# Optimization experiments

Hardware: AMD Instinct MI355X
Metric: run time of the kernel (lower is better)

Reference implementation:

```python
import jax, jax.numpy as jnp
import numpy as np
import math

EPS = 1e-5

def _bn_lrelu(x, g, b, m, v):
    # BatchNorm2d (eval, running stats) + LeakyReLU(0.01)
    inv = jax.lax.rsqrt(v + EPS)
    xn = (x - m[None, :, None, None]) * (g * inv)[None, :, None, None] + b[None, :, None, None]
    return jnp.where(xn >= 0, xn, 0.01 * xn)

def _conv3x3(x, w, b):
    # zero pad 1 on freq (dim2) and time (dim3) (pad_left state is None -> zeros), valid 3x3 conv
    x = jnp.pad(x, ((0, 0), (0, 0), (1, 1), (1, 1)))
    y = jax.lax.conv_general_dilated(x, w, (1, 1), 'VALID',
                                     dimension_numbers=('NCHW', 'OIHW', 'NCHW'))
    return y + b[None, :, None, None]

def _conv1x1(x, w, b):
    return jnp.einsum('bcft,oc->boft', x, w[:, :, 0, 0]) + b[None, :, None, None]

def _blockx3(x, g, b, m, v, w, wb):
    return _conv3x3(_bn_lrelu(x, g, b, m, v), w, wb)

def _mha(x, wqkv, bqkv, wo, bo, n_heads=4, L=64, U=128):
    # banded local attention over time, window = (L back, L fwd), chunked by U
    B, C, F, T = x.shape
    H = n_heads; D = C // H; S = 2 * L
    qkv = _conv1x1(x, wqkv, bqkv)                 # [B,3C,F,T]
    qkv = qkv.transpose(0, 2, 1, 3)               # [B,F,3C,T]
    def split(a):
        return a.reshape(B * F, H, D, T).transpose(0, 1, 3, 2)  # [BF,H,T,D]
    q = split(qkv[:, :, :C])
    k = split(qkv[:, :, C:2 * C])
    v = split(qkv[:, :, 2 * C:])
    Tkv = T + L                                   # kv padded left by L (zero state)
    nC = T // U
    pad_to = nC * U + S                           # pad kv right so every chunk window exists
    kp = jnp.pad(k, ((0, 0), (0, 0), (L, pad_to - Tkv), (0, 0)))
    vp = jnp.pad(v, ((0, 0), (0, 0), (L, pad_to - Tkv), (0, 0)))
    idx = (jnp.arange(nC) * U)[:, None] + jnp.arange(U + S)[None, :]   # [nC, U+S]
    kc = kp[:, :, idx, :]                         # [BF,H,nC,U+S,D]
    vc = vp[:, :, idx, :]
    qc = q.reshape(B * F, H, nC, U, D)
    i = jnp.arange(U)[:, None]; j = jnp.arange(U + S)[None, :]
    band = (j >= i) & (j <= i + S)                # row i sees cols i..i+S (width 1+2L)
    valid = (jnp.arange(nC)[:, None] * U + jnp.arange(U + S)[None, :]) < Tkv
    mask = (band[None, :, :] & valid[:, None, :]).astype(x.dtype)      # [nC,U,U+S]
    scores = jnp.einsum('bhcqd,bhckd->bhcqk', qc, kc) / math.sqrt(D)
    scores = scores * mask - 10000.0 * (1.0 - mask)
    p = jax.nn.softmax(scores, axis=-1)
    o = jnp.einsum('bhcqk,bhckd->bhcqd', p, vc)   # [BF,H,nC,U,D]
    o = o.reshape(B * F, H, T, D).transpose(0, 1, 3, 2).reshape(B, F, C, T).transpose(0, 2, 1, 3)
    return _conv1x1(o, wo, bo)

def setup_inputs() -> dict:
    key = jax.random.key(0)
    ks = jax.random.split(key, 40)
    d = {}
    d['x'] = jax.random.normal(ks[0], (4, 64, 64, 512), dtype=jnp.float32)
    def bn(i, c, pre):
        d[pre + '_g'] = jax.random.normal(ks[i], (c,), jnp.float32) * 0.1 + 1.0
        d[pre + '_b'] = jax.random.normal(ks[i + 1], (c,), jnp.float32) * 0.1
        d[pre + '_m'] = jax.random.normal(ks[i + 2], (c,), jnp.float32) * 0.1
        d[pre + '_v'] = jax.random.uniform(ks[i + 3], (c,), jnp.float32, 0.5, 1.5)
    def conv(i, o, c, kh, kw, pre):
        fan = c * kh * kw
        d[pre + '_w'] = jax.random.normal(ks[i], (o, c, kh, kw), jnp.float32) / math.sqrt(fan)
        d[pre + '_wb'] = jax.random.normal(ks[i + 1], (o,), jnp.float32) * 0.01
    bn(1, 64, 'bd0');  conv(5, 32, 64, 3, 3, 'bd0')
    bn(7, 96, 'bd1');  conv(11, 32, 96, 3, 3, 'bd1')
    bn(13, 128, 'bdo'); conv(17, 64, 128, 3, 3, 'bdo')
    d['qkv_w'] = jax.random.normal(ks[19], (192, 64, 1, 1), jnp.float32) / math.sqrt(64)
    d['qkv_b'] = jax.random.normal(ks[20], (192,), jnp.float32) * 0.01
    d['o_w'] = jax.random.normal(ks[21], (64, 64, 1, 1), jnp.float32) / math.sqrt(64)
    d['o_b'] = jax.random.normal(ks[22], (64,), jnp.float32) * 0.01
    bn(23, 128, 'sao'); conv(27, 64, 128, 1, 1, 'sao')
    return d

def reference(x,
              bd0_g, bd0_b, bd0_m, bd0_v, bd0_w, bd0_wb,
              bd1_g, bd1_b, bd1_m, bd1_v, bd1_w, bd1_wb,
              bdo_g, bdo_b, bdo_m, bdo_v, bdo_w, bdo_wb,
              qkv_w, qkv_b, o_w, o_b,
              sao_g, sao_b, sao_m, sao_v, sao_w, sao_wb):
    # dense conv stack: 64 -> +32 -> +32 -> 64
    a0 = _blockx3(x, bd0_g, bd0_b, bd0_m, bd0_v, bd0_w, bd0_wb)
    x1 = jnp.concatenate([x, a0], axis=1)                 # [B,96,F,T]
    a1 = _blockx3(x1, bd1_g, bd1_b, bd1_m, bd1_v, bd1_w, bd1_wb)
    x2 = jnp.concatenate([x1, a1], axis=1)                # [B,128,F,T]
    y = _blockx3(x2, bdo_g, bdo_b, bdo_m, bdo_v, bdo_w, bdo_wb)  # [B,64,F,T]
    # banded self-attention branch
    att = _mha(y, qkv_w, qkv_b, o_w, o_b)                 # [B,64,F,T]
    z = jnp.concatenate([y, att], axis=1)                 # [B,128,F,T]
    out = _conv1x1(_bn_lrelu(z, sao_g, sao_b, sao_m, sao_v), sao_w, sao_wb)
    return out
```

## Files before the change

kernel.cpp:

```cpp
#include <hip/hip_runtime.h>
#include <hip/hip_bf16.h>

typedef unsigned short u16t;
typedef __attribute__((ext_vector_type(8))) short bfrag;
typedef __attribute__((ext_vector_type(4))) float f32x4;
typedef __attribute__((ext_vector_type(8))) unsigned short uh8;

__device__ __forceinline__ float bfu(u16t u) {
    union { unsigned int i; float f; } c;
    c.i = ((unsigned int)u) << 16;
    return c.f;
}
__device__ __forceinline__ u16t fbf(float f) {
    __hip_bfloat16 h = __float2bfloat16(f);
    return *reinterpret_cast<u16t*>(&h);
}
__device__ __forceinline__ unsigned int fbf2(float lo, float hi) {
    unsigned int r;
    asm("v_cvt_pk_bf16_f32 %0, %1, %2" : "=v"(r) : "v"(lo), "v"(hi));
    return r;
}
__device__ __forceinline__ float rcpf(float x) {
    float r;
    asm("v_rcp_f32 %0, %1" : "=v"(r) : "v"(x));
    return r;
}

__global__ __launch_bounds__(256) void prep_x3_k(
    const float* __restrict__ x,
    const float* __restrict__ g0, const float* __restrict__ b0,
    const float* __restrict__ m0, const float* __restrict__ v0,
    const float* __restrict__ g1, const float* __restrict__ b1,
    const float* __restrict__ m1, const float* __restrict__ v1,
    const float* __restrict__ g2, const float* __restrict__ b2,
    const float* __restrict__ m2, const float* __restrict__ v2,
    u16t* __restrict__ xn0, u16t* __restrict__ xn1, u16t* __restrict__ xn2)
{
    constexpr int F = 64, T = 512;
    __shared__ u16t su[64][74];
    __shared__ float ssc[3][64], ssh[3][64];
    const int tid = threadIdx.x;
    const int t0 = blockIdx.x * 64;
    const int f = blockIdx.y, b = blockIdx.z;

    if (tid < 64) {
        int c = tid;
        float s;
        s = g0[c] * rsqrtf(v0[c] + 1e-5f); ssc[0][c] = s; ssh[0][c] = b0[c] - m0[c] * s;
        s = g1[c] * rsqrtf(v1[c] + 1e-5f); ssc[1][c] = s; ssh[1][c] = b1[c] - m1[c] * s;
        s = g2[c] * rsqrtf(v2[c] + 1e-5f); ssc[2][c] = s; ssh[2][c] = b2[c] - m2[c] * s;
    }
#pragma unroll
    for (int p = 0; p < 16; p++) {
        int i = tid + 256 * p;
        int c = i >> 6, t = i & 63;
        su[c][t] = fbf(x[(((long)b * 64 + c) * F + f) * T + t0 + t]);
    }
    __syncthreads();
#pragma unroll
    for (int p = 0; p < 2; p++) {
        int i = tid + 256 * p;
        int t = i >> 3, c8 = i & 7;
        float n0[8], n1[8], n2[8];
#pragma unroll
        for (int j = 0; j < 8; j++) {
            int c = c8 * 8 + j;
            float xv = bfu(su[c][t]);
            float a0 = fmaf(xv, ssc[0][c], ssh[0][c]);
            float a1 = fmaf(xv, ssc[1][c], ssh[1][c]);
            float a2 = fmaf(xv, ssc[2][c], ssh[2][c]);
            n0[j] = fmaxf(a0, 0.01f * a0);
            n1[j] = fmaxf(a1, 0.01f * a1);
            n2[j] = fmaxf(a2, 0.01f * a2);
        }
        union { uh8 h; unsigned int w[4]; } u0, u1, u2;
#pragma unroll
        for (int j4 = 0; j4 < 4; j4++) {
            u0.w[j4] = fbf2(n0[j4 * 2], n0[j4 * 2 + 1]);
            u1.w[j4] = fbf2(n1[j4 * 2], n1[j4 * 2 + 1]);
            u2.w[j4] = fbf2(n2[j4 * 2], n2[j4 * 2 + 1]);
        }
        long gi = (((long)b * F + f) * T + t0 + t) * 64 + c8 * 8;
        *(uh8*)&xn0[gi] = u0.h;
        *(uh8*)&xn1[gi] = u1.h;
        *(uh8*)&xn2[gi] = u2.h;
    }
}

__global__ __launch_bounds__(256) void prep_w_k(
    const float* __restrict__ w0, const float* __restrict__ w1,
    const float* __restrict__ w2, const float* __restrict__ ow,
    const float* __restrict__ sw, const float* __restrict__ qw,
    u16t* __restrict__ wp)
{
    int idx = blockIdx.x * 256 + threadIdx.x;
    if (idx >= 144384) return;
    if (idx < 119808) {
        int C_IN, C_OUT, e;
        const float* src;
        if (idx < 18432)      { C_IN = 64;  C_OUT = 32; src = w0; e = idx; }
        else if (idx < 46080) { C_IN = 96;  C_OUT = 32; src = w1; e = idx - 18432; }
        else                  { C_IN = 128; C_OUT = 64; src = w2; e = idx - 46080; }
        int NCOT = C_OUT / 16;
        int j  = e & 7;
        int l  = (e >> 3) & 63;
        int r  = e >> 9;
        int ct = r % NCOT;
        int r2 = r / NCOT;
        int kk = r2 % 9;
        int cb = r2 / 9;
        int co  = ct * 16 + (l & 15);
        int kin = cb * 32 + (l >> 4) * 8 + j;
        int kh = kk / 3, kw = kk % 3;
        wp[idx] = fbf(src[((co * C_IN + kin) * 3 + kh) * 3 + kw]);
    } else if (idx < 123904) {
        int e = idx - 119808;
        int ks = e & 31, co = (e >> 5) & 63, kb = e >> 11;
        wp[idx] = fbf(ow[co * 64 + kb * 32 + ks]);
    } else if (idx < 132096) {
        int e = idx - 123904;
        int ks = e & 31, co = (e >> 5) & 63, kb = e >> 11;
        wp[idx] = fbf(sw[co * 128 + kb * 32 + ks]);
    } else {
        int e = idx - 132096;
        int ks = e & 31, co = (e >> 5) % 192, kb = e / 6144;
        wp[idx] = fbf(qw[co * 64 + kb * 32 + ks]);
    }
}

template<int C_IN, int C_OUT, int EPI>
__global__ __launch_bounds__(256) void conv3x3_ff4_k(
    const u16t* __restrict__ s0, const u16t* __restrict__ s1,
    const u16t* __restrict__ s2,
    const u16t* __restrict__ wseg, const float* __restrict__ wb,
    const float* __restrict__ g1, const float* __restrict__ b1,
    const float* __restrict__ m1, const float* __restrict__ v1,
    const float* __restrict__ g2, const float* __restrict__ b2,
    const float* __restrict__ m2, const float* __restrict__ v2,
    int bnoff, u16t* __restrict__ dst1, u16t* __restrict__ dst2)
{
    constexpr int F = 64, T = 512, TT = 64, FF = 4;
    constexpr int NCH  = C_IN / 32;
    constexpr int NCOT = C_OUT / 16;
    constexpr int WT = 9 * NCOT * 64;
    constexpr int XT = 6 * 66 * 4;

    __shared__ __align__(16) u16t s_x[6][66][40];
    __shared__ __align__(16) u16t s_w[WT * 8];

    const int tid = threadIdx.x;
    const int t0 = blockIdx.x * TT;
    const int f0 = blockIdx.y * FF;
    const int b  = blockIdx.z;

    const int l  = tid & 63;
    const int wv = tid >> 6;
    const int lr = l & 15;
    const int lq = l >> 4;

    f32x4 acc[4][NCOT];
#pragma unroll
    for (int i = 0; i < 4; i++)
#pragma unroll
        for (int j = 0; j < NCOT; j++) acc[i][j] = (f32x4){0.f, 0.f, 0.f, 0.f};

    for (int ch = 0; ch < NCH; ch++) {
        if (ch) __syncthreads();

        for (int idx = tid; idx < XT + WT; idx += 256) {
            if (idx < XT) {
                int oct = idx & 3;
                int row = idx >> 2;
                int fr = row / 66;
                int tp = row - fr * 66;
                int fi = f0 + fr - 1;
                int tg = t0 + tp - 1;
                int gc8 = ch * 4 + oct;
                uh8 v = (uh8)0;
                if ((unsigned)fi < (unsigned)F && (unsigned)tg < (unsigned)T) {
                    const u16t* sp; int coff, cw;
                    if (C_IN == 64 || gc8 < 8) { sp = s0; coff = gc8 * 8;        cw = 64; }
                    else if (gc8 < 12)         { sp = s1; coff = (gc8 - 8) * 8;  cw = 32; }
                    else                       { sp = s2; coff = (gc8 - 12) * 8; cw = 32; }
                    v = *(const uh8*)&sp[(((long)b * F + fi) * T + tg) * cw + coff];
                }
                *(uh8*)&s_x[fr][tp][oct * 8] = v;
            } else {
                int w = idx - XT;
                *(uh8*)&s_w[w * 8] = *(const uh8*)&wseg[((long)ch * WT + w) * 8];
            }
        }
        __syncthreads();

#pragma unroll
        for (int kk = 0; kk < 9; kk++) {
            const int kh = kk / 3, kw = kk % 3;
            bfrag A[NCOT];
#pragma unroll
            for (int ct = 0; ct < NCOT; ct++)
                A[ct] = *(const bfrag*)&s_w[((kk * NCOT + ct) * 64 + l) * 8];
#pragma unroll
            for (int ts = 0; ts < 4; ts++) {
                bfrag B = *(const bfrag*)&s_x[wv + kh][ts * 16 + lr + kw][lq * 8];
#pragma unroll
                for (int ct = 0; ct < NCOT; ct++)
                    acc[ts][ct] = __builtin_amdgcn_mfma_f32_16x16x32_bf16(
                        A[ct], B, acc[ts][ct], 0, 0, 0);
            }
        }
    }

    const int f = f0 + wv;
#pragma unroll
    for (int ct = 0; ct < NCOT; ct++) {
        const int co0 = ct * 16 + lq * 4;
        float4 bs = *(const float4*)&wb[co0];
        float sc1[4], sh1[4], sc2[4], sh2[4];
        if (EPI >= 1) {
#pragma unroll
            for (int j = 0; j < 4; j++) {
                int c = bnoff + co0 + j;
                float s = g1[c] * rsqrtf(v1[c] + 1e-5f);
                sc1[j] = s; sh1[j] = b1[c] - m1[c] * s;
            }
        }
        if (EPI == 2) {
#pragma unroll
            for (int j = 0; j < 4; j++) {
                int c = bnoff + co0 + j;
                float s = g2[c] * rsqrtf(v2[c] + 1e-5f);
                sc2[j] = s; sh2[j] = b2[c] - m2[c] * s;
            }
        }
#pragma unroll
        for (int ts = 0; ts < 4; ts++) {
            const int t = t0 + ts * 16 + lr;
            long ob = (((long)b * F + f) * T + t) * C_OUT + co0;
            float a[4];
            a[0] = acc[ts][ct][0] + bs.x;
            a[1] = acc[ts][ct][1] + bs.y;
            a[2] = acc[ts][ct][2] + bs.z;
            a[3] = acc[ts][ct][3] + bs.w;
            if (EPI == 0) {
                uint2 pk;
                pk.x = fbf2(a[0], a[1]);
                pk.y = fbf2(a[2], a[3]);
                *(uint2*)&dst1[ob] = pk;
            } else {
                float n[4];
#pragma unroll
                for (int j = 0; j < 4; j++) {
                    float v = fmaf(a[j], sc1[j], sh1[j]);
                    n[j] = fmaxf(v, 0.01f * v);
                }
                uint2 p1;
                p1.x = fbf2(n[0], n[1]);
                p1.y = fbf2(n[2], n[3]);
                *(uint2*)&dst1[ob] = p1;
                if (EPI == 2) {
#pragma unroll
                    for (int j = 0; j < 4; j++) {
                        float v = fmaf(a[j], sc2[j], sh2[j]);
                        n[j] = fmaxf(v, 0.01f * v);
                    }
                    uint2 p2;
                    p2.x = fbf2(n[0], n[1]);
                    p2.y = fbf2(n[2], n[3]);
                    *(uint2*)&dst2[ob] = p2;
                }
            }
        }
    }
}

__global__ __launch_bounds__(256) void qkv_mfma_k(
    const u16t* __restrict__ ybf, const u16t* __restrict__ wq,
    const float* __restrict__ qbias,
    u16t* __restrict__ q_t, u16t* __restrict__ k_t, u16t* __restrict__ v_t)
{
    constexpr int F = 64, T = 512;
    __shared__ __align__(16) u16t s_y[64][72];
    const int tid = threadIdx.x;
    const int t0 = blockIdx.x * 64;
    const int f = blockIdx.y, b = blockIdx.z;
    const long bf = (long)b * F + f;

    for (int i = tid; i < 512; i += 256) {
        int tt = i >> 3, c0 = (i & 7) * 8;
        *(uh8*)&s_y[tt][c0] = *(const uh8*)&ybf[(bf * T + t0 + tt) * 64 + c0];
    }
    __syncthreads();

    const int l = tid & 63, wv = tid >> 6;
    const int lr = l & 15, lq = l >> 4;
    const int tb = wv * 16 + lr;

    bfrag B0 = *(const bfrag*)&s_y[tb][lq * 8];
    bfrag B1 = *(const bfrag*)&s_y[tb][32 + lq * 8];

    f32x4 acc[12];
#pragma unroll
    for (int i = 0; i < 12; i++) acc[i] = (f32x4){0.f, 0.f, 0.f, 0.f};
#pragma unroll
    for (int ct = 0; ct < 12; ct++) {
        bfrag A0 = *(const bfrag*)&wq[(ct * 16 + lr) * 32 + lq * 8];
        acc[ct] = __builtin_amdgcn_mfma_f32_16x16x32_bf16(A0, B0, acc[ct], 0, 0, 0);
    }
#pragma unroll
    for (int ct = 0; ct < 12; ct++) {
        bfrag A1 = *(const bfrag*)&wq[(192 + ct * 16 + lr) * 32 + lq * 8];
        acc[ct] = __builtin_amdgcn_mfma_f32_16x16x32_bf16(A1, B1, acc[ct], 0, 0, 0);
    }

    const float QS = 0.25f * 1.44269504088896f;
    const int t = t0 + tb;
#pragma unroll
    for (int ct = 0; ct < 12; ct++) {
        int co0 = ct * 16 + lq * 4;
        float4 bi = *(const float4*)&qbias[co0];
        float a0 = acc[ct][0] + bi.x, a1 = acc[ct][1] + bi.y;
        float a2 = acc[ct][2] + bi.z, a3 = acc[ct][3] + bi.w;
        if (co0 < 64) {
            uint2 pk;
            pk.x = fbf2(a0 * QS, a1 * QS);
            pk.y = fbf2(a2 * QS, a3 * QS);
            *(uint2*)&q_t[(bf * T + t) * 64 + co0] = pk;
        } else if (co0 < 128) {
            int hh = (co0 - 64) >> 4, d0 = (co0 - 64) & 15;
            uint2 pk;
            pk.x = fbf2(a0, a1);
            pk.y = fbf2(a2, a3);
            *(uint2*)&k_t[((bf * 4 + hh) * T + t) * 16 + d0] = pk;
        } else {
            int hh = (co0 - 128) >> 4, d0 = (co0 - 128) & 15;
            long vb = (bf * 4 + hh) * 16;
            v_t[(vb + d0 + 0) * T + t] = fbf(a0);
            v_t[(vb + d0 + 1) * T + t] = fbf(a1);
            v_t[(vb + d0 + 2) * T + t] = fbf(a2);
            v_t[(vb + d0 + 3) * T + t] = fbf(a3);
        }
    }
}

__global__ __launch_bounds__(256) void attn_mfma_k(
    const u16t* __restrict__ qt, const u16t* __restrict__ kt_,
    const u16t* __restrict__ vt, u16t* __restrict__ ob)
{
    constexpr int T = 512, F = 64;
    const int qc = blockIdx.x & 7;
    const int h  = blockIdx.x >> 3;
    const int f = blockIdx.y, b = blockIdx.z;
    const int qb0 = qc * 64;
    const int tid = threadIdx.x;
    const long bf = (long)b * F + f;
    const long kvb = bf * 4 + h;

    __shared__ __align__(16) u16t s_p[4][16][168];

    const int l  = tid & 63;
    const int wv = tid >> 6;
    const int lr = l & 15;
    const int lq = l >> 4;
    const int qt0 = qb0 + wv * 16;

    bfrag Bq = (bfrag)0;
    if (lq < 2)
        Bq = *(const bfrag*)&qt[(bf * T + qt0 + lr) * 64 + h * 16 + lq * 8];

    bfrag Kf[9];
    const int pK0 = qt0 - 64 + lr;
#pragma unroll
    for (int kti = 0; kti < 9; kti++) {
        if (lq < 2)
            Kf[kti] = *(const bfrag*)&kt_[(kvb * T + pK0 + kti * 16) * 16 + lq * 8];
        else
            Kf[kti] = (bfrag)0;
    }
    bfrag Vf[5];
    const int pV0 = qb0 - 64 + wv * 16 + lq * 8;
#pragma unroll
    for (int kc = 0; kc < 5; kc++)
        Vf[kc] = *(const bfrag*)&vt[(kvb * 16 + lr) * T + pV0 + kc * 32];

    if (qc == 0) {
#pragma unroll
        for (int kti = 0; kti < 9; kti++)
            if (pK0 + kti * 16 < 0) Kf[kti] = (bfrag)0;
#pragma unroll
        for (int kc = 0; kc < 5; kc++)
            if (pV0 + kc * 32 < 0) Vf[kc] = (bfrag)0;
    }
    if (qc == 7) {
#pragma unroll
        for (int kc = 0; kc < 5; kc++)
            if (pV0 + kc * 32 >= T) Vf[kc] = (bfrag)0;
    }

    f32x4 sf[9];
#pragma unroll
    for (int kti = 0; kti < 9; kti++)
        sf[kti] = __builtin_amdgcn_mfma_f32_16x16x32_bf16(
            Kf[kti], Bq, (f32x4){0.f, 0.f, 0.f, 0.f}, 0, 0, 0);

    if (qc == 7) {
#pragma unroll
        for (int kti = 0; kti < 9; kti++)
#pragma unroll
            for (int j = 0; j < 4; j++) {
                int rk = kti * 16 + lq * 4 + j;
                int dq = rk - lr;
                int p  = qt0 - 64 + rk;
                sf[kti][j] = (dq >= 0 && dq <= 128 && p < T) ? sf[kti][j] : -1.0e30f;
            }
    } else {
#pragma unroll
        for (int j = 0; j < 4; j++) {
            int rk0 = lq * 4 + j;
            if (rk0 < lr)      sf[0][j] = -1.0e30f;
            if (rk0 > lr)      sf[8][j] = -1.0e30f;
        }
    }

    float lsum = 0.f;
#pragma unroll
    for (int kti = 0; kti < 9; kti++)
#pragma unroll
        for (int j = 0; j < 4; j++) {
            float e = exp2f(fminf(sf[kti][j], 120.f));
            sf[kti][j] = e;
            lsum += e;
        }
    lsum += __shfl_xor(lsum, 16);
    lsum += __shfl_xor(lsum, 32);

#pragma unroll
    for (int kti = 0; kti < 9; kti++) {
        uint2 pp;
        pp.x = fbf2(sf[kti][0], sf[kti][1]);
        pp.y = fbf2(sf[kti][2], sf[kti][3]);
        *(uint2*)&s_p[wv][lr][kti * 16 + lq * 4] = pp;
    }
    {
        uint2 z; z.x = 0; z.y = 0;
        *(uint2*)&s_p[wv][lr][144 + lq * 4] = z;
    }
    __syncthreads();

    f32x4 oa = (f32x4){0.f, 0.f, 0.f, 0.f};
#pragma unroll
    for (int kc = 0; kc < 5; kc++) {
        bfrag Bp = *(const bfrag*)&s_p[wv][lr][kc * 32 + lq * 8];
        oa = __builtin_amdgcn_mfma_f32_16x16x32_bf16(Vf[kc], Bp, oa, 0, 0, 0);
    }
    const float inv = rcpf(lsum);
    uint2 ov;
    ov.x = fbf2(oa[0] * inv, oa[1] * inv);
    ov.y = fbf2(oa[2] * inv, oa[3] * inv);
    *(uint2*)&ob[(bf * T + qt0 + lr) * 64 + h * 16 + lq * 4] = ov;
}

__global__ __launch_bounds__(256) void final_mfma_k(
    const u16t* __restrict__ ob, const u16t* __restrict__ yb,
    const u16t* __restrict__ wo, const float* __restrict__ obias,
    const float* __restrict__ sg, const float* __restrict__ sb,
    const float* __restrict__ sm, const float* __restrict__ sv,
    const u16t* __restrict__ wsao, const float* __restrict__ swb,
    float* __restrict__ out)
{
    constexpr int F = 64, T = 512, TT = 64, P = 72;
    __shared__ __align__(16) u16t s_ob[64][P];
    __shared__ __align__(16) u16t s_y2[64][P];
    __shared__ __align__(16) u16t s_att[64][P];
    __shared__ float s_sc[128], s_sh[128];

    const int tid = threadIdx.x;
    const int t0 = blockIdx.x * TT;
    const int f = blockIdx.y, b = blockIdx.z;

    if (tid < 128) {
        float sc = sg[tid] * rsqrtf(sv[tid] + 1e-5f);
        s_sc[tid] = sc;
        s_sh[tid] = sb[tid] - sm[tid] * sc;
    }
    __syncthreads();

    for (int i = tid; i < 512; i += 256) {
        int tt = i >> 3, c0 = (i & 7) * 8;
        long gi = (((long)b * F + f) * T + t0 + tt) * 64 + c0;
        *(uh8*)&s_ob[tt][c0] = *(const uh8*)&ob[gi];
        uh8 raw = *(const uh8*)&yb[gi];
        float n[8];
#pragma unroll
        for (int j = 0; j < 8; j++) {
            float xv = bfu(raw[j]);
            float xn = fmaf(xv, s_sc[c0 + j], s_sh[c0 + j]);
            n[j] = fmaxf(xn, 0.01f * xn);
        }
        union { uh8 h; unsigned int w[4]; } u;
#pragma unroll
        for (int j4 = 0; j4 < 4; j4++) u.w[j4] = fbf2(n[j4 * 2], n[j4 * 2 + 1]);
        *(uh8*)&s_y2[tt][c0] = u.h;
    }
    __syncthreads();

    const int l  = tid & 63;
    const int wv = tid >> 6;
    const int lr = l & 15;
    const int lq = l >> 4;
    const int tbase = wv * 16 + lr;
    const int cbase = lq * 8;

    f32x4 acc1[4];
#pragma unroll
    for (int i = 0; i < 4; i++) acc1[i] = (f32x4){0.f, 0.f, 0.f, 0.f};
#pragma unroll
    for (int kb = 0; kb < 2; kb++) {
        bfrag B = *(const bfrag*)&s_ob[tbase][kb * 32 + cbase];
#pragma unroll
        for (int ct = 0; ct < 4; ct++) {
            bfrag A = *(const bfrag*)&wo[(kb * 64 + ct * 16 + lr) * 32 + lq * 8];
            acc1[ct] = __builtin_amdgcn_mfma_f32_16x16x32_bf16(A, B, acc1[ct], 0, 0, 0);
        }
    }
#pragma unroll
    for (int ct = 0; ct < 4; ct++) {
        int co = ct * 16 + lq * 4;
        float4 bi = *(const float4*)&obias[co];
        float n[4];
#pragma unroll
        for (int j = 0; j < 4; j++) {
            float a = acc1[ct][j] + ((j == 0) ? bi.x : (j == 1) ? bi.y : (j == 2) ? bi.z : bi.w);
            int cg = 64 + co + j;
            float xn = fmaf(a, s_sc[cg], s_sh[cg]);
            n[j] = fmaxf(xn, 0.01f * xn);
        }
        uint2 pk;
        pk.x = fbf2(n[0], n[1]);
        pk.y = fbf2(n[2], n[3]);
        *(uint2*)&s_att[tbase][co] = pk;
    }
    __syncthreads();

    f32x4 acc2[4];
#pragma unroll
    for (int i = 0; i < 4; i++) acc2[i] = (f32x4){0.f, 0.f, 0.f, 0.f};
#pragma unroll
    for (int kb = 0; kb < 4; kb++) {
        bfrag B = (kb < 2) ? *(const bfrag*)&s_y2[tbase][kb * 32 + cbase]
                           : *(const bfrag*)&s_att[tbase][(kb - 2) * 32 + cbase];
#pragma unroll
        for (int ct = 0; ct < 4; ct++) {
            bfrag A = *(const bfrag*)&wsao[(kb * 64 + ct * 16 + lr) * 32 + lq * 8];
            acc2[ct] = __builtin_amdgcn_mfma_f32_16x16x32_bf16(A, B, acc2[ct], 0, 0, 0);
        }
    }
    const int t = t0 + wv * 16 + lr;
#pragma unroll
    for (int ct = 0; ct < 4; ct++) {
        int co0 = ct * 16 + lq * 4;
        float4 bs = *(const float4*)&swb[co0];
#pragma unroll
        for (int j = 0; j < 4; j++) {
            float bv = (j == 0) ? bs.x : (j == 1) ? bs.y : (j == 2) ? bs.z : bs.w;
            out[(((long)b * 64 + co0 + j) * F + f) * T + t] = acc2[ct][j] + bv;
        }
    }
}

extern "C" void kernel_launch(void* const* d_in, const int* in_sizes, int n_in,
                              void* d_out, int out_size, void* d_ws, size_t ws_size,
                              hipStream_t stream)
{
    (void)in_sizes; (void)n_in; (void)out_size; (void)ws_size;

    const float* x      = (const float*)d_in[0];
    const float* bd0_g  = (const float*)d_in[1];
    const float* bd0_b  = (const float*)d_in[2];
    const float* bd0_m  = (const float*)d_in[3];
    const float* bd0_v  = (const float*)d_in[4];
    const float* bd0_w  = (const float*)d_in[5];
    const float* bd0_wb = (const float*)d_in[6];
    const float* bd1_g  = (const float*)d_in[7];
    const float* bd1_b  = (const float*)d_in[8];
    const float* bd1_m  = (const float*)d_in[9];
    const float* bd1_v  = (const float*)d_in[10];
    const float* bd1_w  = (const float*)d_in[11];
    const float* bd1_wb = (const float*)d_in[12];
    const float* bdo_g  = (const float*)d_in[13];
    const float* bdo_b  = (const float*)d_in[14];
    const float* bdo_m  = (const float*)d_in[15];
    const float* bdo_v  = (const float*)d_in[16];
    const float* bdo_w  = (const float*)d_in[17];
    const float* bdo_wb = (const float*)d_in[18];
    const float* qkv_w  = (const float*)d_in[19];
    const float* qkv_b  = (const float*)d_in[20];
    const float* o_w    = (const float*)d_in[21];
    const float* o_b    = (const float*)d_in[22];
    const float* sao_g  = (const float*)d_in[23];
    const float* sao_b  = (const float*)d_in[24];
    const float* sao_m  = (const float*)d_in[25];
    const float* sao_v  = (const float*)d_in[26];
    const float* sao_w  = (const float*)d_in[27];
    const float* sao_wb = (const float*)d_in[28];

    char* ws = (char*)d_ws;
    u16t* xn0  = (u16t*)(ws);
    u16t* xn1  = (u16t*)(ws + 16777216);
    u16t* xn2  = (u16t*)(ws + 33554432);
    u16t* a0n1 = (u16t*)(ws + 50331648);
    u16t* a0n2 = (u16t*)(ws + 58720256);
    u16t* a1n2 = (u16t*)(ws + 67108864);
    u16t* ybf  = xn0;
    u16t* q_t  = xn1;
    u16t* k_t  = xn2;
    u16t* v_t  = a0n1;
    u16t* obf  = q_t;
    u16t* wpk  = (u16t*)(ws + 75497472);

    dim3 blk(256);
    dim3 gprep(8, 64, 4);
    dim3 gconv(8, 16, 4);

    hipLaunchKernelGGL(prep_x3_k, gprep, blk, 0, stream, x,
        bd0_g, bd0_b, bd0_m, bd0_v, bd1_g, bd1_b, bd1_m, bd1_v,
        bdo_g, bdo_b, bdo_m, bdo_v, xn0, xn1, xn2);
    hipLaunchKernelGGL(prep_w_k, dim3(564), blk, 0, stream,
        bd0_w, bd1_w, bdo_w, o_w, sao_w, qkv_w, wpk);
    hipLaunchKernelGGL((conv3x3_ff4_k<64, 32, 2>), gconv, blk, 0, stream,
        xn0, nullptr, nullptr, wpk, bd0_wb,
        bd1_g, bd1_b, bd1_m, bd1_v, bdo_g, bdo_b, bdo_m, bdo_v,
        64, a0n1, a0n2);
    hipLaunchKernelGGL((conv3x3_ff4_k<96, 32, 1>), gconv, blk, 0, stream,
        xn1, a0n1, nullptr, wpk + 18432, bd1_wb,
        bdo_g, bdo_b, bdo_m, bdo_v, nullptr, nullptr, nullptr, nullptr,
        96, a1n2, nullptr);
    hipLaunchKernelGGL((conv3x3_ff4_k<128, 64, 0>), gconv, blk, 0, stream,
        xn2, a0n2, a1n2, wpk + 46080, bdo_wb,
        nullptr, nullptr, nullptr, nullptr, nullptr, nullptr, nullptr, nullptr,
        0, ybf, nullptr);
    hipLaunchKernelGGL(qkv_mfma_k, gprep, blk, 0, stream,
        ybf, wpk + 132096, qkv_b, q_t, k_t, v_t);
    hipLaunchKernelGGL(attn_mfma_k, dim3(32, 64, 4), blk, 0, stream,
        q_t, k_t, v_t, obf);
    hipLaunchKernelGGL(final_mfma_k, gprep, blk, 0, stream,
        obf, ybf, wpk + 119808, o_b, sao_g, sao_b, sao_m, sao_v,
        wpk + 123904, sao_wb, (float*)d_out);
}
```

Before: 178.1 us.

## Store Q/K/V and attention output in MFMA-fragment-tiled per-head layout

Q, K, V and the attention output are now stored per (batch,freq,head) in 16-time by 8-dim tiles that match the MFMA fragment shape, replacing the row-major [t][64] and transposed V layouts. Each lane's fragment load becomes a contiguous 16-byte read within a 256-byte tile, so the attention kernel's global loads coalesce better and the strided V transpose stores go away. The producer, attention and final kernels are all updated for the new indexing. The V boundary masking condition is widened to qc>=6.

Result: no change. 176.9 us, median of 2 (-0.7%).

```diff
diff --git a/kernel.cpp b/kernel.cpp
--- a/kernel.cpp
+++ b/kernel.cpp
@@ -314,6 +314,7 @@
 
     const float QS = 0.25f * 1.44269504088896f;
     const int t = t0 + tb;
+    const long kvbase = bf * 4;
 #pragma unroll
     for (int ct = 0; ct < 12; ct++) {
         int co0 = ct * 16 + lq * 4;
@@ -321,23 +322,29 @@
         float a0 = acc[ct][0] + bi.x, a1 = acc[ct][1] + bi.y;
         float a2 = acc[ct][2] + bi.z, a3 = acc[ct][3] + bi.w;
         if (co0 < 64) {
+            int hh = co0 >> 4, d0 = co0 & 15;
+            long idx = (kvbase + hh) * 8192
+                     + ((t >> 4) * 2 + (d0 >> 3)) * 128 + (t & 15) * 8 + (d0 & 7);
             uint2 pk;
             pk.x = fbf2(a0 * QS, a1 * QS);
             pk.y = fbf2(a2 * QS, a3 * QS);
-            *(uint2*)&q_t[(bf * T + t) * 64 + co0] = pk;
+            *(uint2*)&q_t[idx] = pk;
         } else if (co0 < 128) {
             int hh = (co0 - 64) >> 4, d0 = (co0 - 64) & 15;
+            long idx = (kvbase + hh) * 8192
+                     + ((t >> 4) * 2 + (d0 >> 3)) * 128 + (t & 15) * 8 + (d0 & 7);
             uint2 pk;
             pk.x = fbf2(a0, a1);
             pk.y = fbf2(a2, a3);
-            *(uint2*)&k_t[((bf * 4 + hh) * T + t) * 16 + d0] = pk;
+            *(uint2*)&k_t[idx] = pk;
         } else {
             int hh = (co0 - 128) >> 4, d0 = (co0 - 128) & 15;
-            long vb = (bf * 4 + hh) * 16;
-            v_t[(vb + d0 + 0) * T + t] = fbf(a0);
-            v_t[(vb + d0 + 1) * T + t] = fbf(a1);
-            v_t[(vb + d0 + 2) * T + t] = fbf(a2);
-            v_t[(vb + d0 + 3) * T + t] = fbf(a3);
+            long base = (kvbase + hh) * 8192
+                      + ((t >> 4) * 2 + ((t >> 3) & 1)) * 128 + (t & 7);
+            v_t[base + (d0 + 0) * 8] = fbf(a0);
+            v_t[base + (d0 + 1) * 8] = fbf(a1);
+            v_t[base + (d0 + 2) * 8] = fbf(a2);
+            v_t[base + (d0 + 3) * 8] = fbf(a3);
         }
     }
 }
@@ -363,37 +370,42 @@
     const int lq = l >> 4;
     const int qt0 = qb0 + wv * 16;
 
+    const u16t* qh = qt  + kvb * 8192;
+    const u16t* kh = kt_ + kvb * 8192;
+    const u16t* vh = vt  + kvb * 8192;
+
     bfrag Bq = (bfrag)0;
     if (lq < 2)
-        Bq = *(const bfrag*)&qt[(bf * T + qt0 + lr) * 64 + h * 16 + lq * 8];
+        Bq = *(const bfrag*)&qh[((qt0 >> 4) * 2 + lq) * 128 + lr * 8];
 
     bfrag Kf[9];
-    const int pK0 = qt0 - 64 + lr;
+    const int kt0 = (qt0 - 64) >> 4;
 #pragma unroll
     for (int kti = 0; kti < 9; kti++) {
         if (lq < 2)
-            Kf[kti] = *(const bfrag*)&kt_[(kvb * T + pK0 + kti * 16) * 16 + lq * 8];
+            Kf[kti] = *(const bfrag*)&kh[((kt0 + kti) * 2 + lq) * 128 + lr * 8];
         else
             Kf[kti] = (bfrag)0;
     }
     bfrag Vf[5];
-    const int pV0 = qb0 - 64 + wv * 16 + lq * 8;
-#pragma unroll
-    for (int kc = 0; kc < 5; kc++)
-        Vf[kc] = *(const bfrag*)&vt[(kvb * 16 + lr) * T + pV0 + kc * 32];
+#pragma unroll
+    for (int kc = 0; kc < 5; kc++) {
+        int t16 = kt0 + kc * 2 + (lq >> 1);
+        Vf[kc] = *(const bfrag*)&vh[(t16 * 2 + (lq & 1)) * 128 + lr * 8];
+    }
 
     if (qc == 0) {
 #pragma unroll
         for (int kti = 0; kti < 9; kti++)
-            if (pK0 + kti * 16 < 0) Kf[kti] = (bfrag)0;
+            if (qt0 - 64 + kti * 16 < 0) Kf[kti] = (bfrag)0;
 #pragma unroll
         for (int kc = 0; kc < 5; kc++)
-            if (pV0 + kc * 32 < 0) Vf[kc] = (bfrag)0;
-    }
-    if (qc == 7) {
+            if (qt0 - 64 + kc * 32 + lq * 8 < 0) Vf[kc] = (bfrag)0;
+    }
+    if (qc >= 6) {
 #pragma unroll
         for (int kc = 0; kc < 5; kc++)
-            if (pV0 + kc * 32 >= T) Vf[kc] = (bfrag)0;
+            if (qt0 - 64 + kc * 32 + lq * 8 >= T) Vf[kc] = (bfrag)0;
     }
 
     f32x4 sf[9];
@@ -453,10 +465,14 @@
         oa = __builtin_amdgcn_mfma_f32_16x16x32_bf16(Vf[kc], Bp, oa, 0, 0, 0);
     }
     const float inv = rcpf(lsum);
+    const int d0 = lq * 4;
+    long oidx = kvb * 8192
+              + (((qt0 + lr) >> 4) * 2 + (d0 >> 3)) * 128
+              + ((qt0 + lr) & 15) * 8 + (d0 & 7);
     uint2 ov;
     ov.x = fbf2(oa[0] * inv, oa[1] * inv);
     ov.y = fbf2(oa[2] * inv, oa[3] * inv);
-    *(uint2*)&ob[(bf * T + qt0 + lr) * 64 + h * 16 + lq * 4] = ov;
+    *(uint2*)&ob[oidx] = ov;
 }
 
 __global__ __launch_bounds__(256) void final_mfma_k(
@@ -476,6 +492,7 @@
     const int tid = threadIdx.x;
     const int t0 = blockIdx.x * TT;
     const int f = blockIdx.y, b = blockIdx.z;
+    const long bf = (long)b * F + f;
 
     if (tid < 128) {
         float sc = sg[tid] * rsqrtf(sv[tid] + 1e-5f);
@@ -486,8 +503,11 @@
 
     for (int i = tid; i < 512; i += 256) {
         int tt = i >> 3, c0 = (i & 7) * 8;
-        long gi = (((long)b * F + f) * T + t0 + tt) * 64 + c0;
-        *(uh8*)&s_ob[tt][c0] = *(const uh8*)&ob[gi];
+        int t = t0 + tt;
+        long oi = (bf * 4 + (c0 >> 4)) * 8192
+                + ((t >> 4) * 2 + ((c0 >> 3) & 1)) * 128 + (t & 15) * 8;
+        *(uh8*)&s_ob[tt][c0] = *(const uh8*)&ob[oi];
+        long gi = (bf * T + t) * 64 + c0;
         uh8 raw = *(const uh8*)&yb[gi];
         float n[8];
 #pragma unroll
```
